# Kernel tuning notes

Measured on AMD Instinct MI355X. Metric: run time of the kernel, lower is better.

The kernel has to match this reference:

```python
import jax, jax.numpy as jnp
import numpy as np

N = 100000      # nodes
E = 3200000     # edges (avg degree 32)
NFEAT = 512
HID = 64
NCLASS = 64
ALPHA = 0.1
NITER = 10


def setup_inputs() -> dict:
    key = jax.random.key(0)
    k1, k2, k3, k4, k5 = jax.random.split(key, 5)
    x = jax.random.normal(k1, (N, NFEAT), dtype=jnp.float32)
    edge_index = jax.random.randint(k2, (2, E), 0, N, dtype=jnp.int32)
    edge_weight = jax.random.uniform(k3, (E,), dtype=jnp.float32)
    W1 = jax.random.normal(k4, (NFEAT, HID), dtype=jnp.float32) * 0.05
    W2 = jax.random.normal(k5, (HID, NCLASS), dtype=jnp.float32) * 0.05
    return {"x": x, "edge_index": edge_index, "edge_weight": edge_weight,
            "W1": W1, "W2": W2}


def reference(x, edge_index, edge_weight, W1, W2):
    # _transform_features (eval mode: dropout = identity, bias=False)
    h = jax.nn.relu(x @ W1)            # [N, HID]
    z0 = h @ W2                        # [N, NCLASS]
    src = edge_index[0]
    dst = edge_index[1]
    z = z0
    # APPNP power iteration: z = adj @ z + alpha * z0
    for _ in range(NITER):
        msg = edge_weight[:, None] * z[src]                          # [E, NCLASS]
        z = jax.ops.segment_sum(msg, dst, num_segments=N) + ALPHA * z0
    return jax.nn.log_softmax(z, axis=-1)
```

## Files before the change

### kernel.cpp

```cpp
#include <hip/hip_runtime.h>

#define NN     100000
#define EE     3200000
#define NF     512
#define HIDN   64
#define NCLS   64
#define ALPHA  0.1f

#define CHUNK  512
#define NB     196

typedef unsigned short ushort_t;
typedef unsigned int   uint_t;

__device__ inline ushort_t f2bf(float f)
{
    uint_t u = __float_as_uint(f);
    u += 0x7FFFu + ((u >> 16) & 1u);
    return (ushort_t)(u >> 16);
}
__device__ inline float bf2f(ushort_t b)
{
    return __uint_as_float(((uint_t)b) << 16);
}

template <bool RELU>
__global__ __launch_bounds__(256) void gemm_kernel(
    const float* __restrict__ A, const float* __restrict__ B,
    float* __restrict__ C, int nrows, int K)
{
    const int BK = 16;
    __shared__ float AsT[BK][68];
    __shared__ float Bs [BK][68];

    int tid = threadIdx.x;
    int tx  = tid & 15;
    int ty  = tid >> 4;
    int rowBase = blockIdx.x * 64;

    int arow = tid >> 2;
    int ak   = (tid & 3) * 4;
    int brow = tid >> 4;
    int bcol = (tid & 15) * 4;

    float acc[4][4] = {};

    for (int k0 = 0; k0 < K; k0 += BK) {
        float4 av;
        int gr = rowBase + arow;
        if (gr < nrows) av = *(const float4*)(A + (size_t)gr * K + k0 + ak);
        else            av = make_float4(0.f, 0.f, 0.f, 0.f);
        float4 bv = *(const float4*)(B + (size_t)(k0 + brow) * 64 + bcol);

        __syncthreads();
        AsT[ak + 0][arow] = av.x;
        AsT[ak + 1][arow] = av.y;
        AsT[ak + 2][arow] = av.z;
        AsT[ak + 3][arow] = av.w;
        *(float4*)&Bs[brow][bcol] = bv;
        __syncthreads();

#pragma unroll
        for (int kk = 0; kk < BK; ++kk) {
            float4 a = *(const float4*)&AsT[kk][ty * 4];
            float4 b = *(const float4*)&Bs [kk][tx * 4];
            acc[0][0] = fmaf(a.x, b.x, acc[0][0]);
            acc[0][1] = fmaf(a.x, b.y, acc[0][1]);
            acc[0][2] = fmaf(a.x, b.z, acc[0][2]);
            acc[0][3] = fmaf(a.x, b.w, acc[0][3]);
            acc[1][0] = fmaf(a.y, b.x, acc[1][0]);
            acc[1][1] = fmaf(a.y, b.y, acc[1][1]);
            acc[1][2] = fmaf(a.y, b.z, acc[1][2]);
            acc[1][3] = fmaf(a.y, b.w, acc[1][3]);
            acc[2][0] = fmaf(a.z, b.x, acc[2][0]);
            acc[2][1] = fmaf(a.z, b.y, acc[2][1]);
            acc[2][2] = fmaf(a.z, b.z, acc[2][2]);
            acc[2][3] = fmaf(a.z, b.w, acc[2][3]);
            acc[3][0] = fmaf(a.w, b.x, acc[3][0]);
            acc[3][1] = fmaf(a.w, b.y, acc[3][1]);
            acc[3][2] = fmaf(a.w, b.z, acc[3][2]);
            acc[3][3] = fmaf(a.w, b.w, acc[3][3]);
        }
    }

#pragma unroll
    for (int i = 0; i < 4; ++i) {
        int r = rowBase + ty * 4 + i;
        if (r < nrows) {
            float4 o;
            o.x = acc[i][0]; o.y = acc[i][1]; o.z = acc[i][2]; o.w = acc[i][3];
            if (RELU) {
                o.x = fmaxf(o.x, 0.f); o.y = fmaxf(o.y, 0.f);
                o.z = fmaxf(o.z, 0.f); o.w = fmaxf(o.w, 0.f);
            }
            *(float4*)(C + (size_t)r * 64 + tx * 4) = o;
        }
    }
}

__global__ __launch_bounds__(256) void zero_kernel(int* __restrict__ p, int n)
{
    int i = blockIdx.x * 256 + threadIdx.x;
    if (i < n) p[i] = 0;
}

__global__ __launch_bounds__(256) void count_kernel(const int* __restrict__ dst,
                                                    int* __restrict__ deg)
{
    int e = blockIdx.x * 256 + threadIdx.x;
    if (e < EE) atomicAdd(&deg[dst[e]], 1);
}

__global__ __launch_bounds__(256) void scanA_kernel(const int* __restrict__ deg,
                                                    int* __restrict__ bsum)
{
    int b = blockIdx.x, t = threadIdx.x;
    int i = b * CHUNK + t * 2;
    int v = 0;
    if (i < NN)     v += deg[i];
    if (i + 1 < NN) v += deg[i + 1];
    __shared__ int sm[256];
    sm[t] = v;
    __syncthreads();
    for (int o = 128; o > 0; o >>= 1) {
        if (t < o) sm[t] += sm[t + o];
        __syncthreads();
    }
    if (t == 0) bsum[b] = sm[0];
}

__global__ __launch_bounds__(256) void scanB_kernel(const int* __restrict__ bsum,
                                                    int* __restrict__ bbase,
                                                    int* __restrict__ offs)
{
    int t = threadIdx.x;
    int v = (t < NB) ? bsum[t] : 0;
    __shared__ int sm[256];
    sm[t] = v;
    __syncthreads();
    for (int o = 1; o < 256; o <<= 1) {
        int u = (t >= o) ? sm[t - o] : 0;
        __syncthreads();
        sm[t] += u;
        __syncthreads();
    }
    if (t < NB) bbase[t] = sm[t] - v;
    if (t == 0) offs[NN] = EE;
}

__global__ __launch_bounds__(256) void scanC_kernel(const int* __restrict__ deg,
                                                    const int* __restrict__ bbase,
                                                    int* __restrict__ offs,
                                                    int* __restrict__ cursor)
{
    int b = blockIdx.x, t = threadIdx.x;
    int i0 = b * CHUNK + t * 2;
    int d0 = (i0 < NN)     ? deg[i0]     : 0;
    int d1 = (i0 + 1 < NN) ? deg[i0 + 1] : 0;
    int local = d0 + d1;
    __shared__ int sm[256];
    sm[t] = local;
    __syncthreads();
    for (int o = 1; o < 256; o <<= 1) {
        int u = (t >= o) ? sm[t - o] : 0;
        __syncthreads();
        sm[t] += u;
        __syncthreads();
    }
    int excl = sm[t] - local + bbase[b];
    if (i0 < NN)     { offs[i0]     = excl;      cursor[i0]     = excl;      }
    if (i0 + 1 < NN) { offs[i0 + 1] = excl + d0; cursor[i0 + 1] = excl + d0; }
}

__global__ __launch_bounds__(256) void scatter_kernel(
    const int* __restrict__ src, const int* __restrict__ dst,
    const float* __restrict__ w, int* cursor, int2* __restrict__ csr)
{
    int e = blockIdx.x * 256 + threadIdx.x;
    if (e >= EE) return;
    int d = dst[e];
    int pos = atomicAdd(&cursor[d], 1);
    csr[pos] = make_int2(src[e], __float_as_int(w[e]));
}

__global__ __launch_bounds__(256) void cvt_kernel(const float* __restrict__ z0,
                                                  ushort_t* __restrict__ zb)
{
    int i = (blockIdx.x * 256 + threadIdx.x) * 4;
    if (i >= NN * 64) return;
    float4 v = *(const float4*)(z0 + i);
    ushort4 o;
    o.x = f2bf(v.x); o.y = f2bf(v.y); o.z = f2bf(v.z); o.w = f2bf(v.w);
    *(ushort4*)(zb + i) = o;
}

template <bool LSM>
__global__ __launch_bounds__(256) void propagate_kernel(
    const ushort_t* __restrict__ zin, const float* __restrict__ z0,
    ushort_t* __restrict__ zout_b, float* __restrict__ zout_f,
    const int* __restrict__ offs, const int2* __restrict__ csr)
{
    int gid  = blockIdx.x * 256 + threadIdx.x;
    int node = gid >> 6;
    int lane = gid & 63;
    if (node >= NN) return;

    int beg = offs[node];
    int end = offs[node + 1];
    float acc = 0.f;
    int j = beg;
    for (; j + 8 <= end; j += 8) {
        int2 e0 = csr[j],     e1 = csr[j + 1], e2 = csr[j + 2], e3 = csr[j + 3];
        int2 e4 = csr[j + 4], e5 = csr[j + 5], e6 = csr[j + 6], e7 = csr[j + 7];
        float v0 = bf2f(zin[(size_t)e0.x * 64 + lane]);
        float v1 = bf2f(zin[(size_t)e1.x * 64 + lane]);
        float v2 = bf2f(zin[(size_t)e2.x * 64 + lane]);
        float v3 = bf2f(zin[(size_t)e3.x * 64 + lane]);
        float v4 = bf2f(zin[(size_t)e4.x * 64 + lane]);
        float v5 = bf2f(zin[(size_t)e5.x * 64 + lane]);
        float v6 = bf2f(zin[(size_t)e6.x * 64 + lane]);
        float v7 = bf2f(zin[(size_t)e7.x * 64 + lane]);
        acc = fmaf(__int_as_float(e0.y), v0, acc);
        acc = fmaf(__int_as_float(e1.y), v1, acc);
        acc = fmaf(__int_as_float(e2.y), v2, acc);
        acc = fmaf(__int_as_float(e3.y), v3, acc);
        acc = fmaf(__int_as_float(e4.y), v4, acc);
        acc = fmaf(__int_as_float(e5.y), v5, acc);
        acc = fmaf(__int_as_float(e6.y), v6, acc);
        acc = fmaf(__int_as_float(e7.y), v7, acc);
    }
    for (; j < end; ++j) {
        int2 e = csr[j];
        acc = fmaf(__int_as_float(e.y), bf2f(zin[(size_t)e.x * 64 + lane]), acc);
    }

    float out = fmaf(ALPHA, z0[(size_t)node * 64 + lane], acc);

    if (LSM) {
        float m = out;
#pragma unroll
        for (int o = 32; o > 0; o >>= 1) m = fmaxf(m, __shfl_xor(m, o, 64));
        float e = __expf(out - m);
        float s = e;
#pragma unroll
        for (int o = 32; o > 0; o >>= 1) s += __shfl_xor(s, o, 64);
        zout_f[(size_t)node * 64 + lane] = (out - m) - __logf(s);
    } else {
        zout_b[(size_t)node * 64 + lane] = f2bf(out);
    }
}

extern "C" void kernel_launch(void* const* d_in, const int* in_sizes, int n_in,
                              void* d_out, int out_size, void* d_ws, size_t ws_size,
                              hipStream_t stream)
{
    const float* x  = (const float*)d_in[0];
    const int*   ei = (const int*)  d_in[1];
    const float* ew = (const float*)d_in[2];
    const float* W1 = (const float*)d_in[3];
    const float* W2 = (const float*)d_in[4];
    const int* src = ei;
    const int* dst = ei + EE;

    char* ws = (char*)d_ws;
    size_t off = 0;
    auto alloc = [&](size_t bytes) -> char* {
        char* p = ws + off;
        off += (bytes + 255) & ~(size_t)255;
        return p;
    };

    float*    h     = (float*)   alloc((size_t)NN * HIDN * 4);
    float*    z0    = (float*)   alloc((size_t)NN * NCLS * 4);
    ushort_t* zbA   = (ushort_t*)alloc((size_t)NN * NCLS * 2);
    ushort_t* zbB   = (ushort_t*)alloc((size_t)NN * NCLS * 2);
    int*      deg   = (int*)     alloc((size_t)NN * 4);
    int*      offs  = (int*)     alloc((size_t)(NN + 1) * 4);
    int*      cur_  = (int*)     alloc((size_t)NN * 4);
    int*      bsum  = (int*)     alloc((size_t)NB * 4);
    int*      bbase = (int*)     alloc((size_t)NB * 4);

    int2* csr = (int2*)h;

    gemm_kernel<true ><<<(NN + 63) / 64, 256, 0, stream>>>(x, W1, h, NN, NF);
    gemm_kernel<false><<<(NN + 63) / 64, 256, 0, stream>>>(h, W2, z0, NN, HIDN);

    zero_kernel<<<(NN + 255) / 256, 256, 0, stream>>>(deg, NN);
    count_kernel<<<EE / 256, 256, 0, stream>>>(dst, deg);
    scanA_kernel<<<NB, 256, 0, stream>>>(deg, bsum);
    scanB_kernel<<<1, 256, 0, stream>>>(bsum, bbase, offs);
    scanC_kernel<<<NB, 256, 0, stream>>>(deg, bbase, offs, cur_);
    scatter_kernel<<<EE / 256, 256, 0, stream>>>(src, dst, ew, cur_, csr);

    cvt_kernel<<<(NN * 64 / 4 + 255) / 256, 256, 0, stream>>>(z0, zbA);

    const ushort_t* cur = zbA;
    ushort_t* nxt = zbB;
    for (int it = 0; it < 9; ++it) {
        propagate_kernel<false><<<(NN * 64) / 256, 256, 0, stream>>>(
            cur, z0, nxt, nullptr, offs, csr);
        ushort_t* t = (ushort_t*)cur; cur = nxt; nxt = t;
    }
    propagate_kernel<true><<<(NN * 64) / 256, 256, 0, stream>>>(
        cur, z0, nullptr, (float*)d_out, offs, csr);
}
```

Baseline: 1.608 ms.

## Partition edges by source range per XCD and reduce partial sums

Edges are now bucketed by destination and by source quarter, giving a CSR with four segments per node. Each source quarter is mapped to a pair of XCDs through the block-index modulo 8, so each XCD's L2 only gathers from about a quarter of the bf16 feature table. Partial sums go to bf16 buffers and a separate reduce kernel adds them with alpha*z0. This costs an extra kernel per iteration, extra partial-buffer traffic, bf16 rounding of partials, and reuse of d_out as scratch. A fallback direct path runs if the workspace is too small.

After: 2.355 ms. 1.47x slower.

```diff
diff --git a/kernel.cpp b/kernel.cpp
--- a/kernel.cpp
+++ b/kernel.cpp
@@ -7,8 +7,11 @@
 #define NCLS   64
 #define ALPHA  0.1f
 
-#define CHUNK  512
-#define NB     196
+#define P       4
+#define PSZ     25000
+#define NP      (NN * P)
+#define CHUNK   512
+#define NB2     ((NP + CHUNK - 1) / CHUNK)
 
 typedef unsigned short ushort_t;
 typedef unsigned int   uint_t;
@@ -104,11 +107,15 @@
     if (i < n) p[i] = 0;
 }
 
-__global__ __launch_bounds__(256) void count_kernel(const int* __restrict__ dst,
+__global__ __launch_bounds__(256) void count_kernel(const int* __restrict__ src,
+                                                    const int* __restrict__ dst,
                                                     int* __restrict__ deg)
 {
     int e = blockIdx.x * 256 + threadIdx.x;
-    if (e < EE) atomicAdd(&deg[dst[e]], 1);
+    if (e < EE) {
+        int k = (uint_t)src[e] / PSZ;
+        atomicAdd(&deg[dst[e] * P + k], 1);
+    }
 }
 
 __global__ __launch_bounds__(256) void scanA_kernel(const int* __restrict__ deg,
@@ -117,8 +124,8 @@
     int b = blockIdx.x, t = threadIdx.x;
     int i = b * CHUNK + t * 2;
     int v = 0;
-    if (i < NN)     v += deg[i];
-    if (i + 1 < NN) v += deg[i + 1];
+    if (i < NP)     v += deg[i];
+    if (i + 1 < NP) v += deg[i + 1];
     __shared__ int sm[256];
     sm[t] = v;
     __syncthreads();
@@ -134,9 +141,16 @@
                                                     int* __restrict__ offs)
 {
     int t = threadIdx.x;
-    int v = (t < NB) ? bsum[t] : 0;
+    int v[4];
+    int tot = 0;
+#pragma unroll
+    for (int j = 0; j < 4; ++j) {
+        int idx = t * 4 + j;
+        v[j] = (idx < NB2) ? bsum[idx] : 0;
+        tot += v[j];
+    }
     __shared__ int sm[256];
-    sm[t] = v;
+    sm[t] = tot;
     __syncthreads();
     for (int o = 1; o < 256; o <<= 1) {
         int u = (t >= o) ? sm[t - o] : 0;
@@ -144,8 +158,14 @@
         sm[t] += u;
         __syncthreads();
     }
-    if (t < NB) bbase[t] = sm[t] - v;
-    if (t == 0) offs[NN] = EE;
+    int run = sm[t] - tot;
+#pragma unroll
+    for (int j = 0; j < 4; ++j) {
+        int idx = t * 4 + j;
+        if (idx < NB2) bbase[idx] = run;
+        run += v[j];
+    }
+    if (t == 0) offs[NP] = EE;
 }
 
 __global__ __launch_bounds__(256) void scanC_kernel(const int* __restrict__ deg,
@@ -155,8 +175,8 @@
 {
     int b = blockIdx.x, t = threadIdx.x;
     int i0 = b * CHUNK + t * 2;
-    int d0 = (i0 < NN)     ? deg[i0]     : 0;
-    int d1 = (i0 + 1 < NN) ? deg[i0 + 1] : 0;
+    int d0 = (i0 < NP)     ? deg[i0]     : 0;
+    int d1 = (i0 + 1 < NP) ? deg[i0 + 1] : 0;
     int local = d0 + d1;
     __shared__ int sm[256];
     sm[t] = local;
@@ -168,8 +188,8 @@
         __syncthreads();
     }
     int excl = sm[t] - local + bbase[b];
-    if (i0 < NN)     { offs[i0]     = excl;      cursor[i0]     = excl;      }
-    if (i0 + 1 < NN) { offs[i0 + 1] = excl + d0; cursor[i0 + 1] = excl + d0; }
+    if (i0 < NP)     { offs[i0]     = excl;      cursor[i0]     = excl;      }
+    if (i0 + 1 < NP) { offs[i0 + 1] = excl + d0; cursor[i0 + 1] = excl + d0; }
 }
 
 __global__ __launch_bounds__(256) void scatter_kernel(
@@ -178,35 +198,108 @@
 {
     int e = blockIdx.x * 256 + threadIdx.x;
     if (e >= EE) return;
-    int d = dst[e];
-    int pos = atomicAdd(&cursor[d], 1);
-    csr[pos] = make_int2(src[e], __float_as_int(w[e]));
+    int s = src[e];
+    int k = (uint_t)s / PSZ;
+    int pos = atomicAdd(&cursor[dst[e] * P + k], 1);
+    csr[pos] = make_int2(s, __float_as_int(w[e]));
 }
 
 __global__ __launch_bounds__(256) void cvt_kernel(const float* __restrict__ z0,
-                                                  ushort_t* __restrict__ zb)
+                                                  ushort_t* __restrict__ z0b,
+                                                  ushort_t* __restrict__ zinit)
 {
     int i = (blockIdx.x * 256 + threadIdx.x) * 4;
     if (i >= NN * 64) return;
     float4 v = *(const float4*)(z0 + i);
     ushort4 o;
     o.x = f2bf(v.x); o.y = f2bf(v.y); o.z = f2bf(v.z); o.w = f2bf(v.w);
-    *(ushort4*)(zb + i) = o;
+    *(ushort4*)(z0b + i) = o;
+    *(ushort4*)(zinit + i) = o;
+}
+
+__global__ __launch_bounds__(256) void subpass_kernel(
+    const ushort_t* __restrict__ zin, ushort_t* __restrict__ p01,
+    ushort_t* __restrict__ p23, const int* __restrict__ offs,
+    const int2* __restrict__ csr)
+{
+    int b    = blockIdx.x;
+    int xcd  = b & 7;
+    int k    = xcd >> 1;
+    int sub  = xcd & 1;
+    int bq   = b >> 3;
+    int wid  = threadIdx.x >> 6;
+    int lane = threadIdx.x & 63;
+    int node = (bq * 2 + sub) * 4 + wid;
+
+    int key = node * P + k;
+    int beg = offs[key];
+    int end = offs[key + 1];
+
+    float acc = 0.f;
+    int j = beg;
+    for (; j + 4 <= end; j += 4) {
+        int2 e0 = csr[j], e1 = csr[j + 1], e2 = csr[j + 2], e3 = csr[j + 3];
+        float v0 = bf2f(zin[(size_t)e0.x * 64 + lane]);
+        float v1 = bf2f(zin[(size_t)e1.x * 64 + lane]);
+        float v2 = bf2f(zin[(size_t)e2.x * 64 + lane]);
+        float v3 = bf2f(zin[(size_t)e3.x * 64 + lane]);
+        acc = fmaf(__int_as_float(e0.y), v0, acc);
+        acc = fmaf(__int_as_float(e1.y), v1, acc);
+        acc = fmaf(__int_as_float(e2.y), v2, acc);
+        acc = fmaf(__int_as_float(e3.y), v3, acc);
+    }
+    for (; j < end; ++j) {
+        int2 e = csr[j];
+        acc = fmaf(__int_as_float(e.y), bf2f(zin[(size_t)e.x * 64 + lane]), acc);
+    }
+
+    ushort_t* pout = (k < 2) ? p01 : p23;
+    size_t idx = (size_t)(k & 1) * NN * 64 + (size_t)node * 64 + lane;
+    pout[idx] = f2bf(acc);
 }
 
 template <bool LSM>
-__global__ __launch_bounds__(256) void propagate_kernel(
-    const ushort_t* __restrict__ zin, const float* __restrict__ z0,
-    ushort_t* __restrict__ zout_b, float* __restrict__ zout_f,
-    const int* __restrict__ offs, const int2* __restrict__ csr)
+__global__ __launch_bounds__(256) void reduce_kernel(
+    const ushort_t* __restrict__ p01, const ushort_t* __restrict__ p23,
+    const ushort_t* __restrict__ z0b, ushort_t* __restrict__ zout_b,
+    float* __restrict__ zout_f)
+{
+    int node = blockIdx.x * 4 + (threadIdx.x >> 6);
+    int lane = threadIdx.x & 63;
+    size_t idx = (size_t)node * 64 + lane;
+    const size_t S = (size_t)NN * 64;
+
+    float out = bf2f(p01[idx]) + bf2f(p01[S + idx])
+              + bf2f(p23[idx]) + bf2f(p23[S + idx])
+              + ALPHA * bf2f(z0b[idx]);
+
+    if (LSM) {
+        float m = out;
+#pragma unroll
+        for (int o = 32; o > 0; o >>= 1) m = fmaxf(m, __shfl_xor(m, o, 64));
+        float e = __expf(out - m);
+        float s = e;
+#pragma unroll
+        for (int o = 32; o > 0; o >>= 1) s += __shfl_xor(s, o, 64);
+        zout_f[idx] = (out - m) - __logf(s);
+    } else {
+        zout_b[idx] = f2bf(out);
+    }
+}
+
+template <bool FINAL>
+__global__ __launch_bounds__(256) void direct_kernel(
+    const ushort_t* __restrict__ zin, ushort_t* __restrict__ z0b,
+    ushort_t* __restrict__ zout, const int* __restrict__ offs,
+    const int2* __restrict__ csr)
 {
     int gid  = blockIdx.x * 256 + threadIdx.x;
     int node = gid >> 6;
     int lane = gid & 63;
     if (node >= NN) return;
 
-    int beg = offs[node];
-    int end = offs[node + 1];
+    int beg = offs[node * P];
+    int end = offs[node * P + P];
     float acc = 0.f;
     int j = beg;
     for (; j + 8 <= end; j += 8) {
@@ -234,20 +327,27 @@
         acc = fmaf(__int_as_float(e.y), bf2f(zin[(size_t)e.x * 64 + lane]), acc);
     }
 
-    float out = fmaf(ALPHA, z0[(size_t)node * 64 + lane], acc);
-
-    if (LSM) {
-        float m = out;
-#pragma unroll
-        for (int o = 32; o > 0; o >>= 1) m = fmaxf(m, __shfl_xor(m, o, 64));
-        float e = __expf(out - m);
-        float s = e;
-#pragma unroll
-        for (int o = 32; o > 0; o >>= 1) s += __shfl_xor(s, o, 64);
-        zout_f[(size_t)node * 64 + lane] = (out - m) - __logf(s);
-    } else {
-        zout_b[(size_t)node * 64 + lane] = f2bf(out);
-    }
+    size_t idx = (size_t)node * 64 + lane;
+    float out = fmaf(ALPHA, bf2f(z0b[idx]), acc);
+    if (FINAL) z0b[idx] = f2bf(out);
+    else       zout[idx] = f2bf(out);
+}
+
+__global__ __launch_bounds__(256) void lsm_kernel(const ushort_t* __restrict__ z,
+                                                  float* __restrict__ out)
+{
+    int node = blockIdx.x * 4 + (threadIdx.x >> 6);
+    int lane = threadIdx.x & 63;
+    size_t idx = (size_t)node * 64 + lane;
+    float v = bf2f(z[idx]);
+    float m = v;
+#pragma unroll
+    for (int o = 32; o > 0; o >>= 1) m = fmaxf(m, __shfl_xor(m, o, 64));
+    float e = __expf(v - m);
+    float s = e;
+#pragma unroll
+    for (int o = 32; o > 0; o >>= 1) s += __shfl_xor(s, o, 64);
+    out[idx] = (v - m) - __logf(s);
 }
 
 extern "C" void kernel_launch(void* const* d_in, const int* in_sizes, int n_in,
@@ -270,37 +370,61 @@
         return p;
     };
 
-    float*    h     = (float*)   alloc((size_t)NN * HIDN * 4);
-    float*    z0    = (float*)   alloc((size_t)NN * NCLS * 4);
-    ushort_t* zbA   = (ushort_t*)alloc((size_t)NN * NCLS * 2);
-    ushort_t* zbB   = (ushort_t*)alloc((size_t)NN * NCLS * 2);
-    int*      deg   = (int*)     alloc((size_t)NN * 4);
-    int*      offs  = (int*)     alloc((size_t)(NN + 1) * 4);
-    int*      cur_  = (int*)     alloc((size_t)NN * 4);
-    int*      bsum  = (int*)     alloc((size_t)NB * 4);
-    int*      bbase = (int*)     alloc((size_t)NB * 4);
+    const size_t ZB = (size_t)NN * 64;
+
+    float*    h     = (float*)   alloc(ZB * 4);
+    float*    z0f   = (float*)   alloc(ZB * 4);
+    ushort_t* z0b   = (ushort_t*)alloc(ZB * 2);
+    int*      deg   = (int*)     alloc((size_t)NP * 4);
+    int*      offs  = (int*)     alloc((size_t)(NP + 1) * 4);
+    int*      cur_  = (int*)     alloc((size_t)NP * 4);
+    int*      bsum  = (int*)     alloc((size_t)NB2 * 4);
+    int*      bbase = (int*)     alloc((size_t)NB2 * 4);
+
+    bool partitioned = (off + ZB * 4 + 256) <= ws_size;
+    ushort_t* p23 = partitioned ? (ushort_t*)alloc(ZB * 4) : nullptr;
+    ushort_t* p01 = (ushort_t*)z0f;
 
     int2* csr = (int2*)h;
+    ushort_t* zb0 = (ushort_t*)d_out;
+    ushort_t* zb1 = zb0 + ZB;
 
     gemm_kernel<true ><<<(NN + 63) / 64, 256, 0, stream>>>(x, W1, h, NN, NF);
-    gemm_kernel<false><<<(NN + 63) / 64, 256, 0, stream>>>(h, W2, z0, NN, HIDN);
-
-    zero_kernel<<<(NN + 255) / 256, 256, 0, stream>>>(deg, NN);
-    count_kernel<<<EE / 256, 256, 0, stream>>>(dst, deg);
-    scanA_kernel<<<NB, 256, 0, stream>>>(deg, bsum);
+    gemm_kernel<false><<<(NN + 63) / 64, 256, 0, stream>>>(h, W2, z0f, NN, HIDN);
+
+    zero_kernel<<<(NP + 255) / 256, 256, 0, stream>>>(deg, NP);
+    count_kernel<<<EE / 256, 256, 0, stream>>>(src, dst, deg);
+    scanA_kernel<<<NB2, 256, 0, stream>>>(deg, bsum);
     scanB_kernel<<<1, 256, 0, stream>>>(bsum, bbase, offs);
-    scanC_kernel<<<NB, 256, 0, stream>>>(deg, bbase, offs, cur_);
+    scanC_kernel<<<NB2, 256, 0, stream>>>(deg, bbase, offs, cur_);
     scatter_kernel<<<EE / 256, 256, 0, stream>>>(src, dst, ew, cur_, csr);
 
-    cvt_kernel<<<(NN * 64 / 4 + 255) / 256, 256, 0, stream>>>(z0, zbA);
-
-    const ushort_t* cur = zbA;
-    ushort_t* nxt = zbB;
-    for (int it = 0; it < 9; ++it) {
-        propagate_kernel<false><<<(NN * 64) / 256, 256, 0, stream>>>(
-            cur, z0, nxt, nullptr, offs, csr);
-        ushort_t* t = (ushort_t*)cur; cur = nxt; nxt = t;
-    }
-    propagate_kernel<true><<<(NN * 64) / 256, 256, 0, stream>>>(
-        cur, z0, nullptr, (float*)d_out, offs, csr);
-}
+    cvt_kernel<<<(NN * 64 / 4 + 255) / 256, 256, 0, stream>>>(z0f, z0b, zb0);
+
+    if (partitioned) {
+        const ushort_t* cur = zb0;
+        ushort_t* nxt = zb1;
+        for (int it = 0; it < 10; ++it) {
+            subpass_kernel<<<NN, 256, 0, stream>>>(cur, p01, p23, offs, csr);
+            if (it < 9) {
+                reduce_kernel<false><<<NN / 4, 256, 0, stream>>>(
+                    p01, p23, z0b, nxt, nullptr);
+                ushort_t* t = (ushort_t*)cur; cur = nxt; nxt = t;
+            } else {
+                reduce_kernel<true><<<NN / 4, 256, 0, stream>>>(
+                    p01, p23, z0b, nullptr, (float*)d_out);
+            }
+        }
+    } else {
+        const ushort_t* cur = zb0;
+        ushort_t* nxt = zb1;
+        for (int it = 0; it < 9; ++it) {
+            direct_kernel<false><<<(NN * 64) / 256, 256, 0, stream>>>(
+                cur, z0b, nxt, offs, csr);
+            ushort_t* t = (ushort_t*)cur; cur = nxt; nxt = t;
+        }
+        direct_kernel<true><<<(NN * 64) / 256, 256, 0, stream>>>(
+            cur, z0b, nullptr, offs, csr);
+        lsm_kernel<<<NN / 4, 256, 0, stream>>>(z0b, (float*)d_out);
+    }
+}
```
